# Kernel tuning notes

Measured on AMD Instinct MI355X. Metric: run time of the kernel, lower is better.

The kernel has to match this reference:

```python
import jax, jax.numpy as jnp
import numpy as np

N, FIN, H, FOUT = 4096, 128, 4, 64
NEG_INF = -1e9


def _xavier(key, shape):
    fan_in, fan_out = shape[-2], shape[-1]
    limit = float(np.sqrt(6.0 / (fan_in + fan_out)))
    return jax.random.uniform(key, shape, jnp.float32, -limit, limit)


def setup_inputs() -> dict:
    key = jax.random.key(0)
    ks = jax.random.split(key, 7)
    x = jax.random.normal(ks[0], (N, FIN), jnp.float32)
    u = jax.random.uniform(ks[1], (N, N))
    mask = jnp.where(u < 0.02, 0.0, NEG_INF).astype(jnp.float32)
    idx = jnp.arange(N)
    mask = mask.at[idx, idx].set(0.0)
    proj_param = _xavier(ks[2], (H, FIN, FOUT))          # per-head projection
    score_src = _xavier(ks[3], (H, FOUT, 1))             # scoring_fn_source (IMP1 layout)
    score_tgt = _xavier(ks[4], (H, FOUT, 1))             # scoring_fn_target
    skip_w = _xavier(ks[5], (H * FOUT, FIN))             # skip_proj Linear weight
    bias = jnp.zeros((H * FOUT,), jnp.float32)
    return {"x": x, "mask": mask, "proj_param": proj_param,
            "score_src": score_src, "score_tgt": score_tgt,
            "skip_w": skip_w, "bias": bias}


def reference(x, mask, proj_param, score_src, score_tgt, skip_w, bias):
    # project: [1,N,Fin] @ [H,Fin,Fout] -> [H,N,Fout]
    h = jnp.einsum('nf,hfo->hno', x, proj_param)
    # additive (Bahdanau-style) scores
    s_src = jnp.matmul(h, score_src)                     # [H,N,1]
    s_tgt = jnp.matmul(h, score_tgt)                     # [H,N,1]
    all_scores = jax.nn.leaky_relu(s_src + jnp.swapaxes(s_tgt, 1, 2), 0.2)  # [H,N,N]
    attn = jax.nn.softmax(all_scores + mask[None, :, :], axis=-1)           # [H,N,N]
    # aggregate: [H,N,N] @ [H,N,Fout] -> [N,H,Fout]
    out = jnp.einsum('hnm,hmo->nho', attn, h)
    # skip connection (dims differ: Fin != H*Fout -> use skip_proj)
    out = out + jnp.matmul(x, skip_w.T).reshape(N, H, FOUT)
    out = out.reshape(N, H * FOUT) + bias                # concat heads + bias
    return jax.nn.elu(out)
```

## Files before the change

kernel.cpp:

```cpp
#include <hip/hip_runtime.h>
#include <hip/hip_bf16.h>
#include <math.h>


#define NN   4096
#define FIN  128
#define NH   4
#define FO   64
#define HF   256
#define LIST 192
#define GEMM_BLOCKS 512

typedef unsigned short ushort_t;
typedef unsigned int uint4n __attribute__((ext_vector_type(4)));

__device__ __forceinline__ ushort_t f2bf(float f) {
    __hip_bfloat16 h = __float2bfloat16(f);
    union { __hip_bfloat16 h; ushort_t u; } c; c.h = h; return c.u;
}
__device__ __forceinline__ float bf2f(ushort_t u) {
    union { unsigned int i; float f; } c; c.i = ((unsigned int)u) << 16; return c.f;
}

__global__ __launch_bounds__(256) void k0_gemm(
        const float* __restrict__ x,
        const float* __restrict__ proj,
        const float* __restrict__ skw,
        const float* __restrict__ asrc,
        const float* __restrict__ atgt,
        ushort_t* __restrict__ h2b, float* __restrict__ skip_ws,
        float* __restrict__ src4, float* __restrict__ tgt4) {
    __shared__ float sA[64 * 68];
    __shared__ float sB[64 * 64];
    const int tid = threadIdx.x;
    const int blk = blockIdx.x;

    const int bc = blk >> 6;
    const int i0 = (blk & 63) * 64;
    const int tx = tid & 15, ty = tid >> 4;
    const int r0 = ty << 2, c0 = tx << 2;
    float acc[4][4] = {};

    #pragma unroll
    for (int kb = 0; kb < FIN; kb += 64) {
        if (kb) __syncthreads();
        #pragma unroll
        for (int q = 0; q < 4; q++) {
            int s   = tid + q * 256;
            int row = s >> 4;
            int c4  = (s & 15) << 2;
            float4 v = *(const float4*)(x + (size_t)(i0 + row) * FIN + kb + c4);
            float* d = sA + row * 68 + c4;
            d[0] = v.x; d[1] = v.y; d[2] = v.z; d[3] = v.w;
        }
        if (bc < 4) {
            const float4* src = (const float4*)(proj + (size_t)bc * FIN * FO
                                                + (size_t)kb * FO);
            #pragma unroll
            for (int q = 0; q < 4; q++) {
                int s = tid + q * 256;
                *(float4*)(sB + (size_t)s * 4) = src[s];
            }
        } else {
            const float* sw = skw + (size_t)(bc - 4) * 64 * FIN;
            #pragma unroll
            for (int q = 0; q < 4; q++) {
                int s  = tid + q * 256;
                int c  = s & 63;
                int k4 = (s >> 6) << 2;
                float4 v = *(const float4*)(sw + (size_t)c * FIN + kb + k4);
                sB[(k4 + 0) * 64 + c] = v.x;
                sB[(k4 + 1) * 64 + c] = v.y;
                sB[(k4 + 2) * 64 + c] = v.z;
                sB[(k4 + 3) * 64 + c] = v.w;
            }
        }
        __syncthreads();

        #pragma unroll 2
        for (int k = 0; k < 64; k += 4) {
            alignas(16) float a[4][4];
            alignas(16) float b[4][4];
            #pragma unroll
            for (int rr = 0; rr < 4; rr++)
                *(float4*)a[rr] = *(const float4*)(sA + (r0 + rr) * 68 + k);
            #pragma unroll
            for (int kk = 0; kk < 4; kk++)
                *(float4*)b[kk] = *(const float4*)(sB + (k + kk) * 64 + c0);
            #pragma unroll
            for (int kk = 0; kk < 4; kk++)
                #pragma unroll
                for (int rr = 0; rr < 4; rr++)
                    #pragma unroll
                    for (int cc = 0; cc < 4; cc++)
                        acc[rr][cc] = fmaf(a[rr][kk], b[kk][cc], acc[rr][cc]);
        }
    }

    if (bc < 4) {
        #pragma unroll
        for (int rr = 0; rr < 4; rr++) {
            ushort4 hv;
            hv.x = f2bf(acc[rr][0]); hv.y = f2bf(acc[rr][1]);
            hv.z = f2bf(acc[rr][2]); hv.w = f2bf(acc[rr][3]);
            *(ushort4*)(h2b + (size_t)(i0 + r0 + rr) * HF + bc * 64 + c0) = hv;
        }
        float as[4], at[4];
        #pragma unroll
        for (int cc = 0; cc < 4; cc++) {
            as[cc] = asrc[bc * FO + c0 + cc];
            at[cc] = atgt[bc * FO + c0 + cc];
        }
        #pragma unroll
        for (int rr = 0; rr < 4; rr++) {
            float ps = acc[rr][0] * as[0] + acc[rr][1] * as[1]
                     + acc[rr][2] * as[2] + acc[rr][3] * as[3];
            float pt = acc[rr][0] * at[0] + acc[rr][1] * at[1]
                     + acc[rr][2] * at[2] + acc[rr][3] * at[3];
            #pragma unroll
            for (int off = 8; off >= 1; off >>= 1) {
                ps += __shfl_xor(ps, off, 64);
                pt += __shfl_xor(pt, off, 64);
            }
            if (tx == 0) {
                int i = i0 + r0 + rr;
                src4[(size_t)i * 4 + bc] = ps;
                tgt4[(size_t)i * 4 + bc] = pt;
            }
        }
    } else {
        float* dst = skip_ws + (size_t)i0 * HF + (bc - 4) * 64;
        #pragma unroll
        for (int rr = 0; rr < 4; rr++)
            *(float4*)(dst + (size_t)(r0 + rr) * HF + c0) = *(float4*)acc[rr];
    }
}

__global__ __launch_bounds__(256, 4) void k1_attn(
        const unsigned int* __restrict__ mask,
        const ushort_t* __restrict__ h2b,
        const float* __restrict__ skip_ws,
        const float* __restrict__ src4,
        const float* __restrict__ tgt4,
        const float* __restrict__ bias,
        float* __restrict__ out) {
    __shared__ ushort_t s_j[4][LIST];
    __shared__ uint2    s_rec[4][4][LIST + 1];
    const int tid  = threadIdx.x;
    const int lane = tid & 63, w = tid >> 6;
    const int i    = blockIdx.x * 4 + w;
    const int h    = lane >> 4;
    const int g    = lane & 15;

    const uint4n* mb = (const uint4n*)(mask + (size_t)i * NN);
    uint4n m[16];
    #pragma unroll
    for (int s = 0; s < 16; s++) m[s] = mb[s * 64 + lane];

    const float4 skipv = *(const float4*)(skip_ws + (size_t)i * HF + 4 * lane);
    const float4 bv    = *(const float4*)(bias + 4 * lane);
    const float  sc    = src4[(size_t)i * 4 + h];

    unsigned long long hm = 0ull;
    #pragma unroll
    for (int s = 0; s < 16; s++)
        #pragma unroll
        for (int e = 0; e < 4; e++)
            if ((m[s][e] & 0x7fffffffu) == 0u)
                hm |= 1ull << (s * 4 + e);

    const int cl = __popcll(hm);
    int incl = cl;
    #pragma unroll
    for (int o = 1; o < 64; o <<= 1) {
        int t = __shfl_up(incl, o, 64);
        if (lane >= o) incl += t;
    }
    const int excl = incl - cl;
    int c = __shfl(incl, 63, 64);
    c = c < LIST ? c : LIST;

    {
        int p = excl;
        unsigned long long mm = hm;
        while (mm) {
            int b = __builtin_ctzll(mm);
            mm &= mm - 1;
            if (p < LIST)
                s_j[w][p] = (ushort_t)((b >> 2) * 256 + lane * 4 + (b & 3));
            p++;
        }
    }

    float lsum = 0.f;
    for (int kk = g; kk < c; kk += 16) {
        int j = s_j[w][kk];
        float pv = sc + tgt4[(size_t)j * 4 + h];
        pv = pv > 0.f ? pv : 0.2f * pv;
        pv = __expf(pv);
        uint2 r;
        r.x = __float_as_uint(pv);
        r.y = (unsigned)j << 9;
        s_rec[w][h][kk] = r;
        lsum += pv;
    }
    #pragma unroll
    for (int o = 8; o >= 1; o >>= 1)
        lsum += __shfl_xor(lsum, o, 64);
    const float inv = lsum > 0.f ? 1.0f / lsum : 0.0f;

    const char* hp = (const char*)(h2b + 4 * lane);
    float4 acc = {0.f, 0.f, 0.f, 0.f};
    int kk = 0;
    for (; kk + 3 < c; kk += 4) {
        uint2 r0 = s_rec[w][h][kk + 0];
        uint2 r1 = s_rec[w][h][kk + 1];
        uint2 r2 = s_rec[w][h][kk + 2];
        uint2 r3 = s_rec[w][h][kk + 3];
        ushort4 a0 = *(const ushort4*)(hp + r0.y);
        ushort4 a1 = *(const ushort4*)(hp + r1.y);
        ushort4 a2 = *(const ushort4*)(hp + r2.y);
        ushort4 a3 = *(const ushort4*)(hp + r3.y);
        float p0 = __uint_as_float(r0.x), p1 = __uint_as_float(r1.x);
        float p2 = __uint_as_float(r2.x), p3 = __uint_as_float(r3.x);
        acc.x = fmaf(p0, bf2f(a0.x), acc.x);
        acc.y = fmaf(p0, bf2f(a0.y), acc.y);
        acc.z = fmaf(p0, bf2f(a0.z), acc.z);
        acc.w = fmaf(p0, bf2f(a0.w), acc.w);
        acc.x = fmaf(p1, bf2f(a1.x), acc.x);
        acc.y = fmaf(p1, bf2f(a1.y), acc.y);
        acc.z = fmaf(p1, bf2f(a1.z), acc.z);
        acc.w = fmaf(p1, bf2f(a1.w), acc.w);
        acc.x = fmaf(p2, bf2f(a2.x), acc.x);
        acc.y = fmaf(p2, bf2f(a2.y), acc.y);
        acc.z = fmaf(p2, bf2f(a2.z), acc.z);
        acc.w = fmaf(p2, bf2f(a2.w), acc.w);
        acc.x = fmaf(p3, bf2f(a3.x), acc.x);
        acc.y = fmaf(p3, bf2f(a3.y), acc.y);
        acc.z = fmaf(p3, bf2f(a3.z), acc.z);
        acc.w = fmaf(p3, bf2f(a3.w), acc.w);
    }
    for (; kk < c; kk++) {
        uint2 r0 = s_rec[w][h][kk];
        ushort4 a0 = *(const ushort4*)(hp + r0.y);
        float p0 = __uint_as_float(r0.x);
        acc.x = fmaf(p0, bf2f(a0.x), acc.x);
        acc.y = fmaf(p0, bf2f(a0.y), acc.y);
        acc.z = fmaf(p0, bf2f(a0.z), acc.z);
        acc.w = fmaf(p0, bf2f(a0.w), acc.w);
    }

    float4 vv;
    vv.x = acc.x * inv + skipv.x + bv.x;
    vv.y = acc.y * inv + skipv.y + bv.y;
    vv.z = acc.z * inv + skipv.z + bv.z;
    vv.w = acc.w * inv + skipv.w + bv.w;
    vv.x = vv.x > 0.f ? vv.x : expm1f(vv.x);
    vv.y = vv.y > 0.f ? vv.y : expm1f(vv.y);
    vv.z = vv.z > 0.f ? vv.z : expm1f(vv.z);
    vv.w = vv.w > 0.f ? vv.w : expm1f(vv.w);
    *(float4*)(out + (size_t)i * HF + 4 * lane) = vv;
}

extern "C" void kernel_launch(void* const* d_in, const int* in_sizes, int n_in,
                              void* d_out, int out_size, void* d_ws, size_t ws_size,
                              hipStream_t stream) {
    const float*        x    = (const float*)d_in[0];
    const unsigned int* mask = (const unsigned int*)d_in[1];
    const float*        proj = (const float*)d_in[2];
    const float*        asrc = (const float*)d_in[3];
    const float*        atgt = (const float*)d_in[4];
    const float*        skw  = (const float*)d_in[5];
    const float*        bias = (const float*)d_in[6];
    float*              out  = (float*)d_out;

    char* ws = (char*)d_ws;
    ushort_t* h2b     = (ushort_t*)ws;
    float*    skip_ws = (float*)(ws + (2u << 20));
    float*    src4    = (float*)(ws + (6u << 20));
    float*    tgt4    = (float*)(ws + (6u << 20) + (64u << 10));

    hipLaunchKernelGGL(k0_gemm, dim3(GEMM_BLOCKS), dim3(256), 0, stream,
                       x, proj, skw, asrc, atgt,
                       h2b, skip_ws, src4, tgt4);
    hipLaunchKernelGGL(k1_attn, dim3(NN / 4), dim3(256), 0, stream,
                       mask, h2b, skip_ws, src4, tgt4, bias, out);
}
```

Before: 127.7 us.

## Precompute mask bitmap inside the GEMM kernel to overlap mask scan

Adds mask-scanning blocks to the first kernel, interleaved one GEMM block per five, that read the 64MB float mask and write a compact 16-bit-per-chunk bitmap. The attention kernel then reads this small bitmap instead of streaming the full mask row. The aim is to overlap the dominant mask read with the GEMM work and shorten the attention kernel's critical path. Neighbour index decoding is changed to match the new bit layout, and the bitmap adds an extra workspace write and read.

After: 130.3 us. +2.0%, slower.

```diff
diff --git a/kernel.cpp b/kernel.cpp
--- a/kernel.cpp
+++ b/kernel.cpp
@@ -10,6 +10,7 @@
 #define HF   256
 #define LIST 192
 #define GEMM_BLOCKS 512
+#define SCAN_BLOCKS 2048
 
 typedef unsigned short ushort_t;
 typedef unsigned int uint4n __attribute__((ext_vector_type(4)));
@@ -22,21 +23,57 @@
     union { unsigned int i; float f; } c; c.i = ((unsigned int)u) << 16; return c.f;
 }
 
-__global__ __launch_bounds__(256) void k0_gemm(
+__global__ __launch_bounds__(256) void k01_fused(
         const float* __restrict__ x,
         const float* __restrict__ proj,
         const float* __restrict__ skw,
         const float* __restrict__ asrc,
         const float* __restrict__ atgt,
+        const unsigned int* __restrict__ mask,
         ushort_t* __restrict__ h2b, float* __restrict__ skip_ws,
-        float* __restrict__ src4, float* __restrict__ tgt4) {
+        float* __restrict__ src4, float* __restrict__ tgt4,
+        ushort_t* __restrict__ bm) {
     __shared__ float sA[64 * 68];
     __shared__ float sB[64 * 64];
     const int tid = threadIdx.x;
     const int blk = blockIdx.x;
-
-    const int bc = blk >> 6;
-    const int i0 = (blk & 63) * 64;
+    const int q5  = blk / 5, r5 = blk - q5 * 5;
+
+    if (r5 != 4) {
+        const int lane = tid & 63, w = tid >> 6;
+        const int wid  = (q5 * 4 + r5) * 4 + w;
+        const uint4n* mb = (const uint4n*)mask;
+
+        const int sgA  = wid;
+        const int sgB  = wid + 8192;
+        const uint4n* pa = mb + (size_t)(sgA >> 2) * 1024 + (sgA & 3) * 256;
+        const uint4n* pb = mb + (size_t)(sgB >> 2) * 1024 + (sgB & 3) * 256;
+
+        uint4n va0 = pa[0 * 64 + lane], va1 = pa[1 * 64 + lane];
+        uint4n va2 = pa[2 * 64 + lane], va3 = pa[3 * 64 + lane];
+        uint4n vb0 = pb[0 * 64 + lane], vb1 = pb[1 * 64 + lane];
+        uint4n vb2 = pb[2 * 64 + lane], vb3 = pb[3 * 64 + lane];
+
+        unsigned ha = 0, hb = 0;
+        #pragma unroll
+        for (int e = 0; e < 4; e++) {
+            ha |= ((va0[e] & 0x7fffffffu) == 0u ? 1u : 0u) << (0 * 4 + e);
+            ha |= ((va1[e] & 0x7fffffffu) == 0u ? 1u : 0u) << (1 * 4 + e);
+            ha |= ((va2[e] & 0x7fffffffu) == 0u ? 1u : 0u) << (2 * 4 + e);
+            ha |= ((va3[e] & 0x7fffffffu) == 0u ? 1u : 0u) << (3 * 4 + e);
+            hb |= ((vb0[e] & 0x7fffffffu) == 0u ? 1u : 0u) << (0 * 4 + e);
+            hb |= ((vb1[e] & 0x7fffffffu) == 0u ? 1u : 0u) << (1 * 4 + e);
+            hb |= ((vb2[e] & 0x7fffffffu) == 0u ? 1u : 0u) << (2 * 4 + e);
+            hb |= ((vb3[e] & 0x7fffffffu) == 0u ? 1u : 0u) << (3 * 4 + e);
+        }
+        bm[(size_t)(sgA >> 2) * 256 + (sgA & 3) * 64 + lane] = (ushort_t)ha;
+        bm[(size_t)(sgB >> 2) * 256 + (sgB & 3) * 64 + lane] = (ushort_t)hb;
+        return;
+    }
+
+    const int gb = q5;
+    const int bc = gb >> 6;
+    const int i0 = (gb & 63) * 64;
     const int tx = tid & 15, ty = tid >> 4;
     const int r0 = ty << 2, c0 = tx << 2;
     float acc[4][4] = {};
@@ -136,8 +173,8 @@
     }
 }
 
-__global__ __launch_bounds__(256, 4) void k1_attn(
-        const unsigned int* __restrict__ mask,
+__global__ __launch_bounds__(256, 4) void k2w_attn(
+        const ushort_t* __restrict__ bm,
         const ushort_t* __restrict__ h2b,
         const float* __restrict__ skip_ws,
         const float* __restrict__ src4,
@@ -152,22 +189,17 @@
     const int h    = lane >> 4;
     const int g    = lane & 15;
 
-    const uint4n* mb = (const uint4n*)(mask + (size_t)i * NN);
-    uint4n m[16];
-    #pragma unroll
-    for (int s = 0; s < 16; s++) m[s] = mb[s * 64 + lane];
+    const ushort4 b4 = *(const ushort4*)(bm + (size_t)i * 256 + lane * 4);
 
     const float4 skipv = *(const float4*)(skip_ws + (size_t)i * HF + 4 * lane);
     const float4 bv    = *(const float4*)(bias + 4 * lane);
     const float  sc    = src4[(size_t)i * 4 + h];
 
-    unsigned long long hm = 0ull;
-    #pragma unroll
-    for (int s = 0; s < 16; s++)
-        #pragma unroll
-        for (int e = 0; e < 4; e++)
-            if ((m[s][e] & 0x7fffffffu) == 0u)
-                hm |= 1ull << (s * 4 + e);
+    unsigned long long hm =
+          (unsigned long long)b4.x
+        | ((unsigned long long)b4.y << 16)
+        | ((unsigned long long)b4.z << 32)
+        | ((unsigned long long)b4.w << 48);
 
     const int cl = __popcll(hm);
     int incl = cl;
@@ -184,10 +216,14 @@
         int p = excl;
         unsigned long long mm = hm;
         while (mm) {
-            int b = __builtin_ctzll(mm);
+            int bit = __builtin_ctzll(mm);
             mm &= mm - 1;
-            if (p < LIST)
-                s_j[w][p] = (ushort_t)((b >> 2) * 256 + lane * 4 + (b & 3));
+            if (p < LIST) {
+                int k = lane * 4 + (bit >> 4);
+                int b = bit & 15;
+                s_j[w][p] = (ushort_t)(((k >> 6) << 10) + ((b >> 2) << 8)
+                                       + ((k & 63) << 2) + (b & 3));
+            }
             p++;
         }
     }
@@ -279,10 +315,12 @@
     float*    skip_ws = (float*)(ws + (2u << 20));
     float*    src4    = (float*)(ws + (6u << 20));
     float*    tgt4    = (float*)(ws + (6u << 20) + (64u << 10));
-
-    hipLaunchKernelGGL(k0_gemm, dim3(GEMM_BLOCKS), dim3(256), 0, stream,
-                       x, proj, skw, asrc, atgt,
-                       h2b, skip_ws, src4, tgt4);
-    hipLaunchKernelGGL(k1_attn, dim3(NN / 4), dim3(256), 0, stream,
-                       mask, h2b, skip_ws, src4, tgt4, bias, out);
-}
+    ushort_t* bm      = (ushort_t*)(ws + (8u << 20));
+
+    hipLaunchKernelGGL(k01_fused, dim3(GEMM_BLOCKS + SCAN_BLOCKS), dim3(256),
+                       0, stream,
+                       x, proj, skw, asrc, atgt, mask,
+                       h2b, skip_ws, src4, tgt4, bm);
+    hipLaunchKernelGGL(k2w_attn, dim3(NN / 4), dim3(256), 0, stream,
+                       bm, h2b, skip_ws, src4, tgt4, bias, out);
+}
```
